# Kernel tuning notes

Measured on AMD Instinct MI355X. Metric: run time of the kernel, lower is better.

The kernel has to match this reference:

```python
import jax, jax.numpy as jnp
import numpy as np

EMB = 768
HEADS = 12
HEAD_DIM = EMB // HEADS
LAMBDA_INIT = 0.5
LN_EPS = 1e-5


def _rope_tables(seq_len, head_dim):
    # theta_j = 10000^{-2j/d}, j = 0..d/2-1 (standard RoPE)
    j = jnp.arange(head_dim // 2, dtype=jnp.float32)
    theta = jnp.power(10000.0, -2.0 * j / head_dim)            # [d/2]
    ang = jnp.arange(seq_len, dtype=jnp.float32)[:, None] * theta[None, :]  # [S, d/2]
    return jnp.cos(ang), jnp.sin(ang)


def _apply_rope(x, cos, sin):
    # x: [B, H, S, D]; cos/sin: [S, D/2]; rotate consecutive pairs (2j, 2j+1)
    x1 = x[..., 0::2]
    x2 = x[..., 1::2]
    c = cos[None, None, :, :]
    s = sin[None, None, :, :]
    r1 = x1 * c - x2 * s
    r2 = x1 * s + x2 * c
    return jnp.stack([r1, r2], axis=-1).reshape(x.shape)


def setup_inputs() -> dict:
    key = jax.random.key(0)
    ks = jax.random.split(key, 10)
    B, S, E = 2, 2048, EMB
    sd = 1.0 / np.sqrt(E)
    return {
        "x": jax.random.normal(ks[0], (B, S, E), jnp.float32),
        "Wq": jax.random.normal(ks[1], (E, 2 * E), jnp.float32) * sd,
        "bq": jnp.zeros((2 * E,), jnp.float32),
        "Wk": jax.random.normal(ks[2], (E, 2 * E), jnp.float32) * sd,
        "bk": jnp.zeros((2 * E,), jnp.float32),
        "Wv": jax.random.normal(ks[3], (E, E), jnp.float32) * sd,
        "bv": jnp.zeros((E,), jnp.float32),
        "Wo": jax.random.normal(ks[4], (E, E), jnp.float32) * sd,
        "bo": jnp.zeros((E,), jnp.float32),
        "q_scale": jnp.ones((1, 1, 2 * E), jnp.float32),
        "k_scale": jnp.ones((1, 1, 2 * E), jnp.float32),
        "v_scale": jnp.ones((1, 1, E), jnp.float32),
        "o_scale": jnp.ones((1, 1, E), jnp.float32),
        "lambda_param": jnp.asarray(0.0, jnp.float32),
    }


def reference(x, Wq, bq, Wk, bk, Wv, bv, Wo, bo,
              q_scale, k_scale, v_scale, o_scale, lambda_param):
    B, S, E = x.shape
    H, D = HEADS, HEAD_DIM

    Q = (x @ Wq + bq) * q_scale          # [B, S, 2E]
    K = (x @ Wk + bk) * k_scale          # [B, S, 2E]
    V = (x @ Wv + bv) * v_scale          # [B, S, E]

    Q1, Q2 = jnp.split(Q, 2, axis=-1)
    K1, K2 = jnp.split(K, 2, axis=-1)

    def to_heads(t):  # [B, S, E] -> [B, H, S, D]
        return t.reshape(B, S, H, D).transpose(0, 2, 1, 3)

    Q1, Q2, K1, K2, Vh = map(to_heads, (Q1, Q2, K1, K2, V))

    cos, sin = _rope_tables(S, D)
    Q1, Q2 = _apply_rope(Q1, cos, sin), _apply_rope(Q2, cos, sin)
    K1, K2 = _apply_rope(K1, cos, sin), _apply_rope(K2, cos, sin)

    scale = 1.0 / jnp.sqrt(jnp.asarray(D, jnp.float32))
    p1 = jax.nn.softmax(jnp.einsum("bhqd,bhkd->bhqk", Q1, K1) * scale, axis=-1)
    p2 = jax.nn.softmax(jnp.einsum("bhqd,bhkd->bhqk", Q2, K2) * scale, axis=-1)

    lam = jax.nn.sigmoid(lambda_param)
    ctx = jnp.einsum("bhqk,bhkd->bhqd", p1 - lam * p2, Vh)  # [B, H, S, D]

    # layer_norm over head_dim, no affine params
    mu = jnp.mean(ctx, axis=-1, keepdims=True)
    var = jnp.mean(jnp.square(ctx - mu), axis=-1, keepdims=True)
    ctx = (ctx - mu) * jax.lax.rsqrt(var + LN_EPS)

    ctx = ctx * (1.0 - LAMBDA_INIT)
    ctx = ctx.transpose(0, 2, 1, 3).reshape(B, S, E)
    return (ctx @ Wo + bo) * o_scale
```

## Files before the change

kernel.cpp:

```cpp
#include <hip/hip_runtime.h>
#include <hip/hip_bf16.h>

#define BB 2
#define SS 2048
#define EE 768
#define HH 12
#define DD 64
#define MM (BB*SS)

typedef __bf16 bf16_t;
typedef __bf16 bf16x8 __attribute__((ext_vector_type(8)));
typedef __bf16 bf16x4 __attribute__((ext_vector_type(4)));
typedef float  f32x4  __attribute__((ext_vector_type(4)));

static __device__ __forceinline__ f32x4 mfma16(bf16x8 a, bf16x8 b, f32x4 c) {
    return __builtin_amdgcn_mfma_f32_16x16x32_bf16(a, b, c, 0, 0, 0);
}

static __device__ __forceinline__ void gload_lds16(const bf16_t* g, bf16_t* l) {
    __builtin_amdgcn_global_load_lds(
        (const __attribute__((address_space(1))) void*)g,
        (__attribute__((address_space(3))) void*)l,
        16, 0, 0);
}

__global__ __launch_bounds__(256)
void prep_kernel(const float* __restrict__ x,
                 const float* __restrict__ Wq, const float* __restrict__ Wk,
                 const float* __restrict__ Wv, const float* __restrict__ Wo,
                 bf16_t* __restrict__ xb,
                 bf16_t* __restrict__ WqT, bf16_t* __restrict__ WkT,
                 bf16_t* __restrict__ WvT, bf16_t* __restrict__ WoT,
                 float* __restrict__ ctab, float* __restrict__ stab)
{
    __shared__ float tile[32][33];
    const int bx = blockIdx.x, tid = threadIdx.x;

    if (bx < 1536) {
        int i = (bx * 256 + tid) * 8;
        float4 a = *reinterpret_cast<const float4*>(x + i);
        float4 b = *reinterpret_cast<const float4*>(x + i + 4);
        bf16x8 v;
        v[0] = (bf16_t)a.x; v[1] = (bf16_t)a.y; v[2] = (bf16_t)a.z; v[3] = (bf16_t)a.w;
        v[4] = (bf16_t)b.x; v[5] = (bf16_t)b.y; v[6] = (bf16_t)b.z; v[7] = (bf16_t)b.w;
        *reinterpret_cast<bf16x8*>(xb + i) = v;
        return;
    }
    if (bx < 1792) {
        int t = (bx - 1536) * 256 + tid;
        int s = t >> 5, j = t & 31;
        float theta = exp2f(-(float)j * (13.287712379549449f / 32.0f));
        float ang = (float)s * theta;
        float sn, cs;
        sincosf(ang, &sn, &cs);
        ctab[t] = cs;
        stab[t] = sn;
        return;
    }
    int idx = bx - 1792;
    const float* W; bf16_t* WT; int N;
    if (idx < 1152)      { W = Wq; WT = WqT; N = 1536; }
    else if (idx < 2304) { W = Wk; WT = WkT; N = 1536; idx -= 1152; }
    else if (idx < 2880) { W = Wv; WT = WvT; N = 768;  idx -= 2304; }
    else                 { W = Wo; WT = WoT; N = 768;  idx -= 2880; }
    const int ntiles = N >> 5;
    const int n0 = (idx % ntiles) * 32, k0 = (idx / ntiles) * 32;
    const int tx = tid & 31, ty = tid >> 5;
    #pragma unroll
    for (int r = 0; r < 32; r += 8)
        tile[ty + r][tx] = W[(size_t)(k0 + ty + r) * N + n0 + tx];
    __syncthreads();
    #pragma unroll
    for (int r = 0; r < 32; r += 8)
        WT[(size_t)(n0 + ty + r) * 768 + k0 + tx] = (bf16_t)tile[tx][ty + r];
}

__global__ __launch_bounds__(256)
void gemm_qkv_kernel(const bf16_t* __restrict__ xb,
                     const bf16_t* __restrict__ WqT, const bf16_t* __restrict__ WkT,
                     const bf16_t* __restrict__ WvT,
                     const float* __restrict__ bq, const float* __restrict__ bk,
                     const float* __restrict__ bv,
                     const float* __restrict__ qs, const float* __restrict__ ks,
                     const float* __restrict__ vs,
                     const float* __restrict__ ctab, const float* __restrict__ stab,
                     bf16_t* __restrict__ Qr, bf16_t* __restrict__ Kr, bf16_t* __restrict__ Vt)
{
    __shared__ __align__(16) bf16_t sm[17408];
    bf16_t* As = sm;
    bf16_t* Bs = sm + 8192;
    const int tid = threadIdx.x;
    const int w = tid >> 6, lane = tid & 63, q15 = lane & 15, g = lane >> 4;
    const int m0 = blockIdx.x * 128;
    const int nt = blockIdx.y;

    const bf16_t* Wsrc; const float* bias; const float* scale;
    int nloc0, mode; bf16_t* dstQK = nullptr; float qmul = 1.0f;
    if (nt < 12)      { Wsrc = WqT; bias = bq; scale = qs; nloc0 = nt * 128;        mode = 0; dstQK = Qr;
                        qmul = 0.125f * 1.4426950408889634f; }
    else if (nt < 24) { Wsrc = WkT; bias = bk; scale = ks; nloc0 = (nt - 12) * 128; mode = 0; dstQK = Kr; }
    else              { Wsrc = WvT; bias = bv; scale = vs; nloc0 = (nt - 24) * 128; mode = 1; }

    f32x4 acc[4][4];
    #pragma unroll
    for (int i = 0; i < 4; ++i)
        #pragma unroll
        for (int j = 0; j < 4; ++j)
            acc[i][j] = f32x4{0.f, 0.f, 0.f, 0.f};

    const bf16_t* gA[4]; const bf16_t* gB[4]; bf16_t* lA[4]; bf16_t* lB[4];
    #pragma unroll
    for (int c = 0; c < 4; ++c) {
        int t16 = c * 256 + tid;
        int row = t16 >> 3;
        int sc16 = (t16 & 7) ^ (row & 7);
        gA[c] = &xb[(size_t)(m0 + row) * 768 + sc16 * 8];
        gB[c] = &Wsrc[(size_t)(nloc0 + row) * 768 + sc16 * 8];
        lA[c] = &As[(c * 256 + w * 64) * 8];
        lB[c] = &Bs[(c * 256 + w * 64) * 8];
    }

    const int ar0 = (w >> 1) * 64, bc0 = (w & 1) * 64;
    const int xr = q15 & 7;

    for (int k0 = 0; k0 < 768; k0 += 64) {
        if (k0) __syncthreads();
        #pragma unroll
        for (int c = 0; c < 4; ++c) {
            gload_lds16(gA[c] + k0, lA[c]);
            gload_lds16(gB[c] + k0, lB[c]);
        }
        __syncthreads();
        #pragma unroll
        for (int st = 0; st < 2; ++st) {
            const int cA = ((4 * st + g) ^ xr) * 8;
            bf16x8 af[4], bfr[4];
            #pragma unroll
            for (int i = 0; i < 4; ++i)
                af[i] = *reinterpret_cast<const bf16x8*>(&As[(ar0 + i * 16 + q15) * 64 + cA]);
            #pragma unroll
            for (int j = 0; j < 4; ++j)
                bfr[j] = *reinterpret_cast<const bf16x8*>(&Bs[(bc0 + j * 16 + q15) * 64 + cA]);
            #pragma unroll
            for (int i = 0; i < 4; ++i)
                #pragma unroll
                for (int j = 0; j < 4; ++j)
                    acc[i][j] = mfma16(af[i], bfr[j], acc[i][j]);
        }
    }

    const int mbase = m0 + (w >> 1) * 64;
    const int nbase = nloc0 + (w & 1) * 64;

    if (mode == 1) {
        __syncthreads();
        #pragma unroll
        for (int j = 0; j < 4; ++j) {
            const int nl = (w & 1) * 64 + j * 16 + q15;
            const int n = nloc0 + nl;
            const float bi = bias[n], sc = scale[n];
            #pragma unroll
            for (int i = 0; i < 4; ++i) {
                const int ml = (w >> 1) * 64 + i * 16 + g * 4;
                #pragma unroll
                for (int r = 0; r < 4; ++r)
                    sm[nl * 136 + ml + r] = (bf16_t)((acc[i][j][r] + bi) * sc);
            }
        }
        __syncthreads();
        const int nl = tid >> 1, mh = (tid & 1) * 64;
        const int n = nloc0 + nl, h = n >> 6, d = n & 63;
        const int b = m0 >> 11, sbase = (m0 & 2047) + mh;
        bf16_t* dst = Vt + ((size_t)(b * HH + h) * DD + d) * SS + sbase;
        #pragma unroll
        for (int c = 0; c < 8; ++c)
            *reinterpret_cast<bf16x8*>(dst + c * 8) =
                *reinterpret_cast<const bf16x8*>(&sm[nl * 136 + mh + c * 8]);
        return;
    }

    #pragma unroll
    for (int j = 0; j < 4; ++j) {
        const int n = nbase + j * 16 + q15;
        const float bi = bias[n];
        const float sc = scale[n] * qmul;
        const int br = (n >= 768) ? 1 : 0;
        const int n2 = n - br * 768;
        const int h = n2 >> 6, d = n2 & 63, jj = d >> 1;
        #pragma unroll
        for (int i = 0; i < 4; ++i)
            #pragma unroll
            for (int r = 0; r < 4; ++r) {
                int m = mbase + i * 16 + g * 4 + r;
                int b = m >> 11, s = m & 2047;
                float v = (acc[i][j][r] + bi) * sc;
                float p = __shfl_xor(v, 1);
                float cs = ctab[s * 32 + jj], sn = stab[s * 32 + jj];
                float outv = (d & 1) ? (p * sn + v * cs) : (v * cs - p * sn);
                dstQK[(((size_t)(b * 2 + br) * HH + h) * SS + s) * DD + d] = (bf16_t)outv;
            }
    }
}

__global__ __launch_bounds__(256)
void attn_kernel(const bf16_t* __restrict__ Qr, const bf16_t* __restrict__ Kr,
                 const bf16_t* __restrict__ Vt, const float* __restrict__ lambda_param,
                 bf16_t* __restrict__ ctx)
{
    __shared__ __align__(16) char smem[51200];
    bf16_t* K1v = (bf16_t*)(smem);
    bf16_t* K2v = (bf16_t*)(smem + 16384);
    bf16_t (*Vs)[72] = (bf16_t (*)[72])(smem + 32768);
    float  (*Cb)[68] = (float  (*)[68])(smem);

    const int idlin = blockIdx.x;
    const int work = ((idlin & 7) * 96) + (idlin >> 3);
    const int bh = work >> 5, b = bh / HH, h = bh % HH;
    const int s0 = (work & 31) * 64;
    const int tid = threadIdx.x, w = tid >> 6, lane = tid & 63, q15 = lane & 15, g = lane >> 4;
    const int br = w >> 1, half = w & 1;

    const bf16_t* Qp = Qr + (((size_t)(b * 2 + br) * HH + h) * SS + (s0 + half * 32 + q15)) * DD;
    bf16x8 qf[2][2];
    #pragma unroll
    for (int j = 0; j < 2; ++j)
        #pragma unroll
        for (int st = 0; st < 2; ++st)
            qf[j][st] = *reinterpret_cast<const bf16x8*>(Qp + (size_t)j * 16 * DD + st * 32 + g * 8);

    const bf16_t* K1base = Kr + ((size_t)(b * 2 + 0) * HH + h) * SS * DD;
    const bf16_t* K2base = Kr + ((size_t)(b * 2 + 1) * HH + h) * SS * DD;
    const bf16_t* Vbase  = Vt + ((size_t)b * HH + h) * DD * SS;

    f32x4 lacc[2];
    f32x4 O[2][4];
    #pragma unroll
    for (int j = 0; j < 2; ++j) {
        lacc[j] = f32x4{0.f, 0.f, 0.f, 0.f};
        #pragma unroll
        for (int df = 0; df < 4; ++df)
            O[j][df] = f32x4{0.f, 0.f, 0.f, 0.f};
    }
    bf16x8 onesv;
    #pragma unroll
    for (int e = 0; e < 8; ++e) onesv[e] = (bf16_t)1.0f;

    const int srow = tid >> 3, scol = (tid & 7) * 8;
    const int u0 = (scol & 32) + ((scol & 15) >> 2) * 8 + ((scol >> 4) & 1) * 4;

    const int krow0 = (lane >> 3);
    const int kc16  = lane & 7;

    bf16x8 rV[2];
    #pragma unroll
    for (int ii = 0; ii < 2; ++ii)
        rV[ii] = *reinterpret_cast<const bf16x8*>(&Vbase[(size_t)(srow + ii * 32) * SS + scol]);

    #pragma unroll
    for (int ii = 0; ii < 2; ++ii) {
        int row = w * 16 + ii * 8 + krow0;
        int sc16 = kc16 ^ (row & 7);
        gload_lds16(&K1base[(size_t)row * DD + sc16 * 8], &K1v[(size_t)(w * 16 + ii * 8) * 64]);
        gload_lds16(&K2base[(size_t)row * DD + sc16 * 8], &K2v[(size_t)(w * 16 + ii * 8) * 64]);
    }

    for (int kb = 0; kb < SS; kb += 64) {
        const int cur = (kb >> 6) & 1;
        #pragma unroll
        for (int ii = 0; ii < 2; ++ii) {
            int r2 = cur * 64 + srow + ii * 32;
            bf16x4 lo = __builtin_shufflevector(rV[ii], rV[ii], 0, 1, 2, 3);
            bf16x4 hi = __builtin_shufflevector(rV[ii], rV[ii], 4, 5, 6, 7);
            *reinterpret_cast<bf16x4*>(&Vs[r2][u0])     = lo;
            *reinterpret_cast<bf16x4*>(&Vs[r2][u0 + 8]) = hi;
        }
        __syncthreads();

        if (kb + 64 < SS) {
            int kn = kb + 64;
            const int nxt = cur ^ 1;
            #pragma unroll
            for (int ii = 0; ii < 2; ++ii) {
                int row = w * 16 + ii * 8 + krow0;
                int sc16 = kc16 ^ (row & 7);
                gload_lds16(&K1base[(size_t)(kn + row) * DD + sc16 * 8],
                            &K1v[((size_t)nxt * 64 + w * 16 + ii * 8) * 64]);
                gload_lds16(&K2base[(size_t)(kn + row) * DD + sc16 * 8],
                            &K2v[((size_t)nxt * 64 + w * 16 + ii * 8) * 64]);
                rV[ii] = *reinterpret_cast<const bf16x8*>(
                    &Vbase[(size_t)(srow + ii * 32) * SS + kn + scol]);
            }
        }

        const bf16_t* Kvb = (br ? K2v : K1v) + (size_t)cur * 64 * 64;
        const bf16_t (*Vsb)[72] = Vs + cur * 64;

        f32x4 sf[2][4];
        #pragma unroll
        for (int rf = 0; rf < 4; ++rf) {
            const bf16_t* krow = &Kvb[(size_t)(rf * 16 + q15) * 64];
            bf16x8 kf0 = *reinterpret_cast<const bf16x8*>(&krow[((g)     ^ (q15 & 7)) * 8]);
            bf16x8 kf1 = *reinterpret_cast<const bf16x8*>(&krow[((4 + g) ^ (q15 & 7)) * 8]);
            #pragma unroll
            for (int j = 0; j < 2; ++j) {
                f32x4 a = mfma16(kf0, qf[j][0], f32x4{0.f, 0.f, 0.f, 0.f});
                sf[j][rf] = mfma16(kf1, qf[j][1], a);
            }
        }

        bf16x8 pa[2][2];
        #pragma unroll
        for (int j = 0; j < 2; ++j)
            #pragma unroll
            for (int st = 0; st < 2; ++st)
                #pragma unroll
                for (int e = 0; e < 8; ++e)
                    pa[j][st][e] = (bf16_t)__builtin_amdgcn_exp2f(sf[j][st * 2 + (e >> 2)][e & 3]);

        #pragma unroll
        for (int j = 0; j < 2; ++j) {
            lacc[j] = mfma16(pa[j][0], onesv, lacc[j]);
            lacc[j] = mfma16(pa[j][1], onesv, lacc[j]);
        }

        #pragma unroll
        for (int df = 0; df < 4; ++df) {
            bf16x8 vf0 = *reinterpret_cast<const bf16x8*>(&Vsb[df * 16 + q15][g * 8]);
            bf16x8 vf1 = *reinterpret_cast<const bf16x8*>(&Vsb[df * 16 + q15][32 + g * 8]);
            #pragma unroll
            for (int j = 0; j < 2; ++j) {
                O[j][df] = mfma16(pa[j][0], vf0, O[j][df]);
                O[j][df] = mfma16(pa[j][1], vf1, O[j][df]);
            }
        }
    }

    __syncthreads();

    if (br == 1) {
        const float lam = 1.0f / (1.0f + __expf(-lambda_param[0]));
        #pragma unroll
        for (int j = 0; j < 2; ++j) {
            #pragma unroll
            for (int r = 0; r < 4; ++r) {
                float inv = lam / lacc[j][r];
                int lq = half * 32 + j * 16 + g * 4 + r;
                #pragma unroll
                for (int df = 0; df < 4; ++df)
                    Cb[lq][df * 16 + q15] = O[j][df][r] * inv;
            }
        }
    }
    __syncthreads();

    if (br == 0) {
        #pragma unroll
        for (int j = 0; j < 2; ++j) {
            #pragma unroll
            for (int r = 0; r < 4; ++r) {
                float inv = 1.0f / lacc[j][r];
                int lq = half * 32 + j * 16 + g * 4 + r;
                float cv[4];
                #pragma unroll
                for (int df = 0; df < 4; ++df)
                    cv[df] = O[j][df][r] * inv - Cb[lq][df * 16 + q15];
                float sum = cv[0] + cv[1] + cv[2] + cv[3];
                sum += __shfl_xor(sum, 1); sum += __shfl_xor(sum, 2);
                sum += __shfl_xor(sum, 4); sum += __shfl_xor(sum, 8);
                float mu = sum * (1.0f / 64.0f);
                float vac = 0.f;
                #pragma unroll
                for (int df = 0; df < 4; ++df) { float dv = cv[df] - mu; vac += dv * dv; }
                vac += __shfl_xor(vac, 1); vac += __shfl_xor(vac, 2);
                vac += __shfl_xor(vac, 4); vac += __shfl_xor(vac, 8);
                float rs = rsqrtf(vac * (1.0f / 64.0f) + 1e-5f);
                int s = s0 + lq;
                size_t rowoff = ((size_t)b * SS + s) * EE + h * DD;
                #pragma unroll
                for (int df = 0; df < 4; ++df)
                    ctx[rowoff + df * 16 + q15] = (bf16_t)((cv[df] - mu) * rs * 0.5f);
            }
        }
    }
}

__global__ __launch_bounds__(256)
void gemm_out_kernel(const bf16_t* __restrict__ ctxb, const bf16_t* __restrict__ WoT,
                     const float* __restrict__ bo, const float* __restrict__ os,
                     float* __restrict__ out)
{
    __shared__ __align__(16) bf16_t As[64 * 64];
    __shared__ __align__(16) bf16_t Bs[128 * 64];
    const int tid = threadIdx.x;
    const int w = tid >> 6, lane = tid & 63, q15 = lane & 15, g = lane >> 4;
    const int m0 = blockIdx.x * 64;
    const int nloc0 = blockIdx.y * 128;

    f32x4 acc[2][4];
    #pragma unroll
    for (int i = 0; i < 2; ++i)
        #pragma unroll
        for (int j = 0; j < 4; ++j)
            acc[i][j] = f32x4{0.f, 0.f, 0.f, 0.f};

    const bf16_t* gA[2]; const bf16_t* gB[4]; bf16_t* lA[2]; bf16_t* lB[4];
    #pragma unroll
    for (int c = 0; c < 2; ++c) {
        int t16 = c * 256 + tid;
        int row = t16 >> 3;
        int sc16 = (t16 & 7) ^ (row & 7);
        gA[c] = &ctxb[(size_t)(m0 + row) * 768 + sc16 * 8];
        lA[c] = &As[(c * 256 + w * 64) * 8];
    }
    #pragma unroll
    for (int c = 0; c < 4; ++c) {
        int t16 = c * 256 + tid;
        int row = t16 >> 3;
        int sc16 = (t16 & 7) ^ (row & 7);
        gB[c] = &WoT[(size_t)(nloc0 + row) * 768 + sc16 * 8];
        lB[c] = &Bs[(c * 256 + w * 64) * 8];
    }

    const int ar0 = (w >> 1) * 32, bc0 = (w & 1) * 64;
    const int xr = q15 & 7;

    for (int k0 = 0; k0 < 768; k0 += 64) {
        if (k0) __syncthreads();
        #pragma unroll
        for (int c = 0; c < 2; ++c) gload_lds16(gA[c] + k0, lA[c]);
        #pragma unroll
        for (int c = 0; c < 4; ++c) gload_lds16(gB[c] + k0, lB[c]);
        __syncthreads();
        #pragma unroll
        for (int st = 0; st < 2; ++st) {
            const int cA = ((4 * st + g) ^ xr) * 8;
            bf16x8 af[2], bfr[4];
            #pragma unroll
            for (int i = 0; i < 2; ++i)
                af[i] = *reinterpret_cast<const bf16x8*>(&As[(ar0 + i * 16 + q15) * 64 + cA]);
            #pragma unroll
            for (int j = 0; j < 4; ++j)
                bfr[j] = *reinterpret_cast<const bf16x8*>(&Bs[(bc0 + j * 16 + q15) * 64 + cA]);
            #pragma unroll
            for (int i = 0; i < 2; ++i)
                #pragma unroll
                for (int j = 0; j < 4; ++j)
                    acc[i][j] = mfma16(af[i], bfr[j], acc[i][j]);
        }
    }

    const int mbase = m0 + (w >> 1) * 32;
    const int nbase = nloc0 + (w & 1) * 64;
    #pragma unroll
    for (int j = 0; j < 4; ++j) {
        const int n = nbase + j * 16 + q15;
        const float bi = bo[n], sc = os[n];
        #pragma unroll
        for (int i = 0; i < 2; ++i)
            #pragma unroll
            for (int r = 0; r < 4; ++r) {
                int m = mbase + i * 16 + g * 4 + r;
                out[(size_t)m * 768 + n] = (acc[i][j][r] + bi) * sc;
            }
    }
}

extern "C" void kernel_launch(void* const* d_in, const int* in_sizes, int n_in,
                              void* d_out, int out_size, void* d_ws, size_t ws_size,
                              hipStream_t stream)
{
    (void)in_sizes; (void)n_in; (void)out_size; (void)ws_size;
    const float* x  = (const float*)d_in[0];
    const float* Wq = (const float*)d_in[1];
    const float* bq = (const float*)d_in[2];
    const float* Wk = (const float*)d_in[3];
    const float* bk = (const float*)d_in[4];
    const float* Wv = (const float*)d_in[5];
    const float* bv = (const float*)d_in[6];
    const float* Wo = (const float*)d_in[7];
    const float* bo = (const float*)d_in[8];
    const float* qs = (const float*)d_in[9];
    const float* ks = (const float*)d_in[10];
    const float* vs = (const float*)d_in[11];
    const float* os = (const float*)d_in[12];
    const float* lp = (const float*)d_in[13];
    float* out = (float*)d_out;

    char* ws = (char*)d_ws;
    bf16_t* xb   = (bf16_t*)(ws);
    bf16_t* WqT  = (bf16_t*)(ws + 6291456);
    bf16_t* WkT  = (bf16_t*)(ws + 8650752);
    bf16_t* WvT  = (bf16_t*)(ws + 11010048);
    bf16_t* WoT  = (bf16_t*)(ws + 12189696);
    bf16_t* Qr   = (bf16_t*)(ws + 13369344);
    bf16_t* Kr   = (bf16_t*)(ws + 25952256);
    bf16_t* Vt   = (bf16_t*)(ws + 38535168);
    bf16_t* ctxb = (bf16_t*)(ws + 44826624);
    float*  ctab = (float*)(ws + 51118080);
    float*  stab = (float*)(ws + 51380224);

    prep_kernel<<<dim3(5248), dim3(256), 0, stream>>>(x, Wq, Wk, Wv, Wo,
                                                      xb, WqT, WkT, WvT, WoT, ctab, stab);
    gemm_qkv_kernel<<<dim3(32, 30), dim3(256), 0, stream>>>(xb, WqT, WkT, WvT,
                                                            bq, bk, bv, qs, ks, vs,
                                                            ctab, stab, Qr, Kr, Vt);
    attn_kernel<<<dim3(768), dim3(256), 0, stream>>>(Qr, Kr, Vt, lp, ctxb);
    gemm_out_kernel<<<dim3(64, 6), dim3(256), 0, stream>>>(ctxb, WoT, bo, os, out);
}
```

Baseline: 125.7 us.

## Pre-permute V in QKV epilogue and load V tiles via async global-to-LDS

The QKV GEMM epilogue now writes V with its in-row column permutation already applied. The attention kernel can then fetch V tiles directly into LDS with global_load_lds, using the same XOR swizzle as K, instead of going through registers and manual LDS stores. This removes register staging and VALU store work from the attention inner loop and trims LDS usage. In exchange, the epilogue issues smaller 8-byte scattered global stores.

Measured after the change: 124.9 us. No clear change (-0.7%).

```diff
diff --git a/kernel.cpp b/kernel.cpp
--- a/kernel.cpp
+++ b/kernel.cpp
@@ -84,7 +84,7 @@
                      const float* __restrict__ qs, const float* __restrict__ ks,
                      const float* __restrict__ vs,
                      const float* __restrict__ ctab, const float* __restrict__ stab,
-                     bf16_t* __restrict__ Qr, bf16_t* __restrict__ Kr, bf16_t* __restrict__ Vt)
+                     bf16_t* __restrict__ Qr, bf16_t* __restrict__ Kr, bf16_t* __restrict__ Vp)
 {
     __shared__ __align__(16) bf16_t sm[17408];
     bf16_t* As = sm;
@@ -171,11 +171,14 @@
         const int nl = tid >> 1, mh = (tid & 1) * 64;
         const int n = nloc0 + nl, h = n >> 6, d = n & 63;
         const int b = m0 >> 11, sbase = (m0 & 2047) + mh;
-        bf16_t* dst = Vt + ((size_t)(b * HH + h) * DD + d) * SS + sbase;
-        #pragma unroll
-        for (int c = 0; c < 8; ++c)
-            *reinterpret_cast<bf16x8*>(dst + c * 8) =
-                *reinterpret_cast<const bf16x8*>(&sm[nl * 136 + mh + c * 8]);
+        bf16_t* dst = Vp + ((size_t)(b * HH + h) * DD + d) * SS + sbase;
+        #pragma unroll
+        for (int c = 0; c < 8; ++c) {
+            const int bc = (c >> 2) * 32 + ((c * 2) & 3) * 8 + ((c >> 1) & 1) * 4;
+            bf16x8 v = *reinterpret_cast<const bf16x8*>(&sm[nl * 136 + mh + c * 8]);
+            *reinterpret_cast<bf16x4*>(dst + bc)     = __builtin_shufflevector(v, v, 0, 1, 2, 3);
+            *reinterpret_cast<bf16x4*>(dst + bc + 8) = __builtin_shufflevector(v, v, 4, 5, 6, 7);
+        }
         return;
     }
 
@@ -204,13 +207,13 @@
 
 __global__ __launch_bounds__(256)
 void attn_kernel(const bf16_t* __restrict__ Qr, const bf16_t* __restrict__ Kr,
-                 const bf16_t* __restrict__ Vt, const float* __restrict__ lambda_param,
+                 const bf16_t* __restrict__ Vp, const float* __restrict__ lambda_param,
                  bf16_t* __restrict__ ctx)
 {
-    __shared__ __align__(16) char smem[51200];
+    __shared__ __align__(16) char smem[49152];
     bf16_t* K1v = (bf16_t*)(smem);
     bf16_t* K2v = (bf16_t*)(smem + 16384);
-    bf16_t (*Vs)[72] = (bf16_t (*)[72])(smem + 32768);
+    bf16_t* Vv  = (bf16_t*)(smem + 32768);
     float  (*Cb)[68] = (float  (*)[68])(smem);
 
     const int idlin = blockIdx.x;
@@ -230,7 +233,7 @@
 
     const bf16_t* K1base = Kr + ((size_t)(b * 2 + 0) * HH + h) * SS * DD;
     const bf16_t* K2base = Kr + ((size_t)(b * 2 + 1) * HH + h) * SS * DD;
-    const bf16_t* Vbase  = Vt + ((size_t)b * HH + h) * DD * SS;
+    const bf16_t* Vbase  = Vp + ((size_t)b * HH + h) * DD * SS;
 
     f32x4 lacc[2];
     f32x4 O[2][4];
@@ -245,35 +248,23 @@
     #pragma unroll
     for (int e = 0; e < 8; ++e) onesv[e] = (bf16_t)1.0f;
 
-    const int srow = tid >> 3, scol = (tid & 7) * 8;
-    const int u0 = (scol & 32) + ((scol & 15) >> 2) * 8 + ((scol >> 4) & 1) * 4;
-
     const int krow0 = (lane >> 3);
     const int kc16  = lane & 7;
-
-    bf16x8 rV[2];
-    #pragma unroll
-    for (int ii = 0; ii < 2; ++ii)
-        rV[ii] = *reinterpret_cast<const bf16x8*>(&Vbase[(size_t)(srow + ii * 32) * SS + scol]);
 
     #pragma unroll
     for (int ii = 0; ii < 2; ++ii) {
         int row = w * 16 + ii * 8 + krow0;
         int sc16 = kc16 ^ (row & 7);
-        gload_lds16(&K1base[(size_t)row * DD + sc16 * 8], &K1v[(size_t)(w * 16 + ii * 8) * 64]);
-        gload_lds16(&K2base[(size_t)row * DD + sc16 * 8], &K2v[(size_t)(w * 16 + ii * 8) * 64]);
+        bf16_t* ldst = (bf16_t*)0;
+        int lrow = (w * 16 + ii * 8) * 64;
+        gload_lds16(&K1base[(size_t)row * DD + sc16 * 8], &K1v[lrow]);
+        gload_lds16(&K2base[(size_t)row * DD + sc16 * 8], &K2v[lrow]);
+        gload_lds16(&Vbase[(size_t)row * SS + sc16 * 8],  &Vv[lrow]);
+        (void)ldst;
     }
 
     for (int kb = 0; kb < SS; kb += 64) {
         const int cur = (kb >> 6) & 1;
-        #pragma unroll
-        for (int ii = 0; ii < 2; ++ii) {
-            int r2 = cur * 64 + srow + ii * 32;
-            bf16x4 lo = __builtin_shufflevector(rV[ii], rV[ii], 0, 1, 2, 3);
-            bf16x4 hi = __builtin_shufflevector(rV[ii], rV[ii], 4, 5, 6, 7);
-            *reinterpret_cast<bf16x4*>(&Vs[r2][u0])     = lo;
-            *reinterpret_cast<bf16x4*>(&Vs[r2][u0 + 8]) = hi;
-        }
         __syncthreads();
 
         if (kb + 64 < SS) {
@@ -283,17 +274,15 @@
             for (int ii = 0; ii < 2; ++ii) {
                 int row = w * 16 + ii * 8 + krow0;
                 int sc16 = kc16 ^ (row & 7);
-                gload_lds16(&K1base[(size_t)(kn + row) * DD + sc16 * 8],
-                            &K1v[((size_t)nxt * 64 + w * 16 + ii * 8) * 64]);
-                gload_lds16(&K2base[(size_t)(kn + row) * DD + sc16 * 8],
-                            &K2v[((size_t)nxt * 64 + w * 16 + ii * 8) * 64]);
-                rV[ii] = *reinterpret_cast<const bf16x8*>(
-                    &Vbase[(size_t)(srow + ii * 32) * SS + kn + scol]);
-            }
-        }
-
-        const bf16_t* Kvb = (br ? K2v : K1v) + (size_t)cur * 64 * 64;
-        const bf16_t (*Vsb)[72] = Vs + cur * 64;
+                int lrow = (nxt * 64 + w * 16 + ii * 8) * 64;
+                gload_lds16(&K1base[(size_t)(kn + row) * DD + sc16 * 8], &K1v[lrow]);
+                gload_lds16(&K2base[(size_t)(kn + row) * DD + sc16 * 8], &K2v[lrow]);
+                gload_lds16(&Vbase[(size_t)row * SS + kn + sc16 * 8],    &Vv[lrow]);
+            }
+        }
+
+        const bf16_t* Kvb = (br ? K2v : K1v) + (size_t)cur * 4096;
+        const bf16_t* Vvb = Vv + (size_t)cur * 4096;
 
         f32x4 sf[2][4];
         #pragma unroll
@@ -325,8 +314,9 @@
 
         #pragma unroll
         for (int df = 0; df < 4; ++df) {
-            bf16x8 vf0 = *reinterpret_cast<const bf16x8*>(&Vsb[df * 16 + q15][g * 8]);
-            bf16x8 vf1 = *reinterpret_cast<const bf16x8*>(&Vsb[df * 16 + q15][32 + g * 8]);
+            const bf16_t* vrow = &Vvb[(size_t)(df * 16 + q15) * 64];
+            bf16x8 vf0 = *reinterpret_cast<const bf16x8*>(&vrow[((g)     ^ (q15 & 7)) * 8]);
+            bf16x8 vf1 = *reinterpret_cast<const bf16x8*>(&vrow[((4 + g) ^ (q15 & 7)) * 8]);
             #pragma unroll
             for (int j = 0; j < 2; ++j) {
                 O[j][df] = mfma16(pa[j][0], vf0, O[j][df]);
@@ -494,7 +484,7 @@
     bf16_t* WoT  = (bf16_t*)(ws + 12189696);
     bf16_t* Qr   = (bf16_t*)(ws + 13369344);
     bf16_t* Kr   = (bf16_t*)(ws + 25952256);
-    bf16_t* Vt   = (bf16_t*)(ws + 38535168);
+    bf16_t* Vp   = (bf16_t*)(ws + 38535168);
     bf16_t* ctxb = (bf16_t*)(ws + 44826624);
     float*  ctab = (float*)(ws + 51118080);
     float*  stab = (float*)(ws + 51380224);
@@ -503,7 +493,7 @@
                                                       xb, WqT, WkT, WvT, WoT, ctab, stab);
     gemm_qkv_kernel<<<dim3(32, 30), dim3(256), 0, stream>>>(xb, WqT, WkT, WvT,
                                                             bq, bk, bv, qs, ks, vs,
-                                                            ctab, stab, Qr, Kr, Vt);
-    attn_kernel<<<dim3(768), dim3(256), 0, stream>>>(Qr, Kr, Vt, lp, ctxb);
+                                                            ctab, stab, Qr, Kr, Vp);
+    attn_kernel<<<dim3(768), dim3(256), 0, stream>>>(Qr, Kr, Vp, lp, ctxb);
     gemm_out_kernel<<<dim3(64, 6), dim3(256), 0, stream>>>(ctxb, WoT, bo, os, out);
 }
```
